# Performance work log

Hardware: AMD Instinct MI355X
Metric: run time of the kernel (lower is better)

## Reference

```python
import jax, jax.numpy as jnp
import numpy as np
import math

ANCHORS = np.array([[[10,13],[16,30],[33,23]],
                    [[30,61],[62,45],[59,119]],
                    [[116,90],[156,198],[373,326]]], dtype=np.float32)
STRIDES = [8.0, 16.0, 32.0]
BALANCE = [4.0, 1.0, 0.4]
LAMBDA_BOX, LAMBDA_OBJ, LAMBDA_CLS = 0.05, 1.0, 0.5
ANCHOR_T = 4.0
CP, CN = 1.0, 0.0  # label_smoothing = 0
EPS = 1e-7


def _bce(x, t):
    # BCEWithLogits, elementwise, numerically stable
    return jnp.maximum(x, 0.) - x * t + jnp.log1p(jnp.exp(-jnp.abs(x)))


def _ciou(b1, b2):
    # b1, b2: (M, 4) xyxy
    ix1 = jnp.maximum(b1[:, 0], b2[:, 0]); iy1 = jnp.maximum(b1[:, 1], b2[:, 1])
    ix2 = jnp.minimum(b1[:, 2], b2[:, 2]); iy2 = jnp.minimum(b1[:, 3], b2[:, 3])
    inter = jnp.clip(ix2 - ix1, 0.) * jnp.clip(iy2 - iy1, 0.)
    a1 = (b1[:, 2] - b1[:, 0]) * (b1[:, 3] - b1[:, 1])
    a2 = (b2[:, 2] - b2[:, 0]) * (b2[:, 3] - b2[:, 1])
    union = a1 + a2 - inter + EPS
    iou = inter / union
    ex1 = jnp.minimum(b1[:, 0], b2[:, 0]); ey1 = jnp.minimum(b1[:, 1], b2[:, 1])
    ex2 = jnp.maximum(b1[:, 2], b2[:, 2]); ey2 = jnp.maximum(b1[:, 3], b2[:, 3])
    c2 = (ex2 - ex1) ** 2 + (ey2 - ey1) ** 2 + EPS
    # center distance^2: centers are (x1+x2)/2
    rho2 = ((b1[:, 0] + b1[:, 2] - b2[:, 0] - b2[:, 2]) ** 2 +
            (b1[:, 1] + b1[:, 3] - b2[:, 1] - b2[:, 3]) ** 2) / 4.
    w1 = b1[:, 2] - b1[:, 0]; h1 = b1[:, 3] - b1[:, 1]
    w2 = b2[:, 2] - b2[:, 0]; h2 = b2[:, 3] - b2[:, 1]
    v = (4. / math.pi ** 2) * (jnp.arctan(w2 / (h2 + EPS)) - jnp.arctan(w1 / (h1 + EPS))) ** 2
    alpha = jax.lax.stop_gradient(v / (1. - iou + v + EPS))  # torch.no_grad()
    return iou - rho2 / c2 - alpha * v


def _layer_loss(pred, targets, anchor, balance):
    # pred: (B, na, H, W, 5+nc); targets: (nt, 6); anchor: (na, 2) in grid units
    B, na, H, W, C = pred.shape
    nc = C - 5
    nt = targets.shape[0]
    gain = jnp.array([1., 1., W, H, W, H], jnp.float32)
    t = targets * gain  # (nt, 6): [b, cls, gx, gy, gw, gh]
    # anchor-ratio filter
    r = t[:, 4:6][None] / (anchor[:, None] + 1e-16)            # (na, nt, 2)
    anchor_ok = jnp.max(jnp.maximum(r, 1. / r), axis=2) < ANCHOR_T  # (na, nt)
    # neighbor-cell selection masks (center + 4 neighbors)
    gxy = t[:, 2:4]
    gxi = jnp.floor(gxy)
    frac = gxy - gxi
    jm = (frac[:, 0] > .5) & (gxi[:, 0] < W - 1)
    km = (frac[:, 1] > .5) & (gxi[:, 1] < H - 1)
    lm = (frac[:, 0] < .5) & (gxi[:, 0] > 0)
    mm = (frac[:, 1] < .5) & (gxi[:, 1] > 0)
    sel = jnp.stack([jnp.ones_like(jm), jm, km, lm, mm])       # (5, nt)
    valid = sel[:, None, :] & anchor_ok[None]                  # (5, na, nt)
    off = jnp.array([[0, 0], [1, 0], [0, 1], [-1, 0], [0, -1]], jnp.float32)
    gxy_e = gxy[None] - off[:, None]                           # (5, nt, 2)
    gi = jnp.clip(jnp.floor(gxy_e).astype(jnp.int32), 0,
                  jnp.array([W - 1, H - 1], jnp.int32))        # (5, nt, 2)
    txy = gxy_e - gi.astype(jnp.float32)                       # offset-form xy
    gwh = t[:, 4:6]
    tbox = jnp.concatenate([txy - gwh[None] / 2., txy + gwh[None] / 2.], -1)  # (5, nt, 4)
    # flatten fixed-size candidate set (5 * na * nt), masked by `valid`
    shp = (5, na, nt)
    b_idx = jnp.broadcast_to(t[:, 0].astype(jnp.int32)[None, None], shp).reshape(-1)
    cls_i = jnp.broadcast_to(t[:, 1].astype(jnp.int32)[None, None], shp).reshape(-1)
    a_idx = jnp.broadcast_to(jnp.arange(na)[None, :, None], shp).reshape(-1)
    gx = jnp.broadcast_to(gi[:, None, :, 0], shp).reshape(-1)
    gy = jnp.broadcast_to(gi[:, None, :, 1], shp).reshape(-1)
    tbox_f = jnp.broadcast_to(tbox[:, None], shp + (4,)).reshape(-1, 4)
    vmask = valid.reshape(-1).astype(pred.dtype)
    cnt = vmask.sum()
    # fancy-indexed gather of matched predictions
    pm = pred[b_idx, a_idx, gy, gx]                            # (M, C)
    pxy = jax.nn.sigmoid(pm[:, :2]) * 2. - 0.5
    pwh = (jax.nn.sigmoid(pm[:, 2:4]) * 2.) ** 2 * anchor[a_idx]
    pbox = jnp.concatenate([pxy - pwh / 2., pxy + pwh / 2.], -1)
    ciou = _ciou(pbox, tbox_f)
    lbox = jnp.where(cnt > 0, jnp.sum((1. - ciou) * vmask) / jnp.maximum(cnt, 1.), 0.)
    # objectness target scatter (detached, clamped CIoU); invalid write 0 -> no-op under max
    tobj = jnp.zeros(pred.shape[:4], pred.dtype)
    vals = jax.lax.stop_gradient(jnp.clip(ciou, 0.) * vmask)
    tobj = tobj.at[b_idx, a_idx, gy, gx].max(vals)
    lobj = jnp.mean(_bce(pred[..., 4], tobj)) * balance
    # classification (mean over matched rows x nc elems)
    ct = CN + (CP - CN) * jax.nn.one_hot(cls_i, nc, dtype=pm.dtype)
    lcls = jnp.where(cnt > 0,
                     jnp.sum(_bce(pm[:, 5:], ct) * vmask[:, None]) / jnp.maximum(cnt * nc, 1.),
                     0.)
    return lbox, lobj, lcls


def _forward(pred0, pred1, pred2, targets):
    B = pred0.shape[0]
    preds = [pred0, pred1, pred2]
    lb = lo = lc = 0.
    for i in range(3):
        anchor = jnp.asarray(ANCHORS[i]) / STRIDES[i]
        bx, ob, cl = _layer_loss(preds[i], targets, anchor, BALANCE[i])
        lb = lb + bx; lo = lo + ob; lc = lc + cl
    return (LAMBDA_BOX * lb + LAMBDA_OBJ * lo + LAMBDA_CLS * lc) * B


def setup_inputs() -> dict:
    key = jax.random.key(0)
    ks = jax.random.split(key, 7)
    B, NT = 16, 300
    pred0 = jax.random.normal(ks[0], (B, 3, 80, 80, 85), jnp.float32)
    pred1 = jax.random.normal(ks[1], (B, 3, 40, 40, 85), jnp.float32)
    pred2 = jax.random.normal(ks[2], (B, 3, 20, 20, 85), jnp.float32)
    b = jax.random.randint(ks[3], (NT, 1), 0, B).astype(jnp.float32)
    c = jax.random.randint(ks[4], (NT, 1), 0, 80).astype(jnp.float32)
    cxy = jax.random.uniform(ks[5], (NT, 2), jnp.float32, 0.02, 0.98)
    wh = jax.random.uniform(ks[6], (NT, 2), jnp.float32, 0.02, 0.3)
    targets = jnp.concatenate([b, c, cxy, wh], axis=1)  # (NT, 6)
    return {"pred0": pred0, "pred1": pred1, "pred2": pred2, "targets": targets}


def reference(pred0, pred1, pred2, targets):
    return _forward(pred0, pred1, pred2, targets)
```

## Files before the change

kernel.cpp:

```cpp
#include <hip/hip_runtime.h>
#include <math.h>

#define EPSF 1e-7f
#define NT1 256
#define NT2 1024

__device__ __constant__ float d_anch[3][3][2] = {
    {{10.f/8.f,  13.f/8.f},  {16.f/8.f,  30.f/8.f},  {33.f/8.f,  23.f/8.f}},
    {{30.f/16.f, 61.f/16.f}, {62.f/16.f, 45.f/16.f}, {59.f/16.f, 119.f/16.f}},
    {{116.f/32.f,90.f/32.f}, {156.f/32.f,198.f/32.f},{373.f/32.f,326.f/32.f}},
};

__device__ __forceinline__ float bce0(float x) {
    return fmaxf(x, 0.0f) + log1pf(expf(-fabsf(x)));
}
__device__ __forceinline__ float bcef(float x, float t) {
    return fmaxf(x, 0.0f) - x * t + log1pf(expf(-fabsf(x)));
}
__device__ __forceinline__ float sigm(float x) {
    return 1.0f / (1.0f + expf(-x));
}

template <int NT>
__device__ __forceinline__ float block_reduce(float v, float* s) {
    s[threadIdx.x] = v;
    __syncthreads();
    for (int st = NT / 2; st > 0; st >>= 1) {
        if (threadIdx.x < st) s[threadIdx.x] += s[threadIdx.x + st];
        __syncthreads();
    }
    float r = s[0];
    __syncthreads();
    return r;
}

__global__ void stream_kernel(const float* __restrict__ pred0,
                              const float* __restrict__ pred1,
                              const float* __restrict__ pred2,
                              float* __restrict__ tobj,
                              float* __restrict__ objpart,
                              int n0, int n1, int n2)
{
    int idx = blockIdx.x * NT1 + threadIdx.x;
    int N = n0 + n1 + n2;
    float acc = 0.0f;
    if (idx < N) {
        tobj[idx] = 0.0f;
        const float* pred; int cell; float w;
        if (idx < n0)           { pred = pred0; cell = idx;            w = 4.0f / (float)n0; }
        else if (idx < n0 + n1) { pred = pred1; cell = idx - n0;       w = 1.0f / (float)n1; }
        else                    { pred = pred2; cell = idx - n0 - n1;  w = 0.4f / (float)n2; }
        float x = pred[(size_t)cell * 85 + 4];
        acc = w * bce0(x);
    }
    __shared__ float s[NT1];
    float r = block_reduce<NT1>(acc, s);
    if (threadIdx.x == 0) objpart[blockIdx.x] = r;
}

__global__ void entry_kernel(const float* __restrict__ pred0,
                             const float* __restrict__ pred1,
                             const float* __restrict__ pred2,
                             const float* __restrict__ targets,
                             int nt, int bpl2,
                             float* __restrict__ tobj_base,
                             float* __restrict__ blockpart,
                             int n0, int n1, int n2)
{
    int layer = blockIdx.x / bpl2;
    int sub   = blockIdx.x % bpl2;
    int wid   = threadIdx.x >> 6;
    int lane  = threadIdx.x & 63;
    int perLayer = 15 * nt;
    int eL = sub * 16 + wid;

    const float* pred; float* tobj; int H, W; float wl;
    if (layer == 0)      { pred = pred0; tobj = tobj_base;           H = 80; W = 80; wl = 4.0f / (float)n0; }
    else if (layer == 1) { pred = pred1; tobj = tobj_base + n0;      H = 40; W = 40; wl = 1.0f / (float)n1; }
    else                 { pred = pred2; tobj = tobj_base + n0 + n1; H = 20; W = 20; wl = 0.4f / (float)n2; }

    float lbox = 0.0f, cnt = 0.0f, corr = 0.0f, clsacc = 0.0f;

    if (eL < perLayer) {
        int t = eL % nt;
        int a = (eL / nt) % 3;
        int o = eL / (nt * 3);

        const float* tg = targets + t * 6;
        float tb = tg[0], tc = tg[1];
        float gx = tg[2] * (float)W, gy = tg[3] * (float)H;
        float gw = tg[4] * (float)W, gh = tg[5] * (float)H;

        float aw = d_anch[layer][a][0], ah = d_anch[layer][a][1];
        float rw = gw / (aw + 1e-16f), rh = gh / (ah + 1e-16f);
        float rmax = fmaxf(fmaxf(rw, 1.0f / rw), fmaxf(rh, 1.0f / rh));
        bool aok = rmax < 4.0f;

        float fxi = floorf(gx), fyi = floorf(gy);
        float fx = gx - fxi, fy = gy - fyi;
        bool selo;
        switch (o) {
            case 0: selo = true; break;
            case 1: selo = (fx > 0.5f) && (fxi < (float)(W - 1)); break;
            case 2: selo = (fy > 0.5f) && (fyi < (float)(H - 1)); break;
            case 3: selo = (fx < 0.5f) && (fxi > 0.0f); break;
            default: selo = (fy < 0.5f) && (fyi > 0.0f); break;
        }

        if (aok && selo) {
            float ox = (o == 1) ? 1.0f : (o == 3) ? -1.0f : 0.0f;
            float oy = (o == 2) ? 1.0f : (o == 4) ? -1.0f : 0.0f;
            float gex = gx - ox, gey = gy - oy;
            int gix = min(max((int)floorf(gex), 0), W - 1);
            int giy = min(max((int)floorf(gey), 0), H - 1);
            float txc = gex - (float)gix, tyc = gey - (float)giy;
            float tx1 = txc - gw * 0.5f, ty1 = tyc - gh * 0.5f;
            float tx2 = txc + gw * 0.5f, ty2 = tyc + gh * 0.5f;

            int b = (int)tb, cls = (int)tc;
            int cell = (int)(((((size_t)b * 3 + a) * H + giy) * W + gix));
            const float* pm = pred + (size_t)cell * 85;

            float p0 = pm[0], p1v = pm[1], p2v = pm[2], p3 = pm[3];
            float pxc = sigm(p0) * 2.0f - 0.5f;
            float pyc = sigm(p1v) * 2.0f - 0.5f;
            float sw = sigm(p2v) * 2.0f;
            float sh = sigm(p3) * 2.0f;
            float pw = sw * sw * aw, ph = sh * sh * ah;
            float px1 = pxc - pw * 0.5f, py1 = pyc - ph * 0.5f;
            float px2 = pxc + pw * 0.5f, py2 = pyc + ph * 0.5f;

            float ix1 = fmaxf(px1, tx1), iy1 = fmaxf(py1, ty1);
            float ix2 = fminf(px2, tx2), iy2 = fminf(py2, ty2);
            float inter = fmaxf(ix2 - ix1, 0.0f) * fmaxf(iy2 - iy1, 0.0f);
            float a1 = (px2 - px1) * (py2 - py1);
            float a2 = (tx2 - tx1) * (ty2 - ty1);
            float uni = a1 + a2 - inter + EPSF;
            float iou = inter / uni;
            float ex1 = fminf(px1, tx1), ey1 = fminf(py1, ty1);
            float ex2 = fmaxf(px2, tx2), ey2 = fmaxf(py2, ty2);
            float cw = ex2 - ex1, chh = ey2 - ey1;
            float c2 = cw * cw + chh * chh + EPSF;
            float dx = px1 + px2 - tx1 - tx2;
            float dy = py1 + py2 - ty1 - ty2;
            float rho2 = (dx * dx + dy * dy) * 0.25f;
            float w1 = px2 - px1, h1 = py2 - py1;
            float w2 = tx2 - tx1, h2 = ty2 - ty1;
            float dat = atanf(w2 / (h2 + EPSF)) - atanf(w1 / (h1 + EPSF));
            float v = 0.40528473f * dat * dat;
            float alpha = v / (1.0f - iou + v + EPSF);
            float ciou = iou - rho2 / c2 - alpha * v;

            if (lane == 0) {
                lbox = 1.0f - ciou;
                cnt = 1.0f;
                float vobj = fmaxf(ciou, 0.0f);
                unsigned int oldb = atomicMax((unsigned int*)&tobj[cell],
                                              __float_as_uint(vobj));
                float old = __uint_as_float(oldb);
                float nw = fmaxf(vobj, old);
                corr = wl * pm[4] * (nw - old);
            }

            float xc = pm[5 + lane];
            clsacc = bcef(xc, (lane == cls) ? 1.0f : 0.0f);
            if (lane < 16) {
                float xc2 = pm[69 + lane];
                clsacc += bcef(xc2, ((64 + lane) == cls) ? 1.0f : 0.0f);
            }
        }
    }

    __shared__ float s[NT2];
    float rb = block_reduce<NT2>(lbox, s);
    float rc = block_reduce<NT2>(cnt, s);
    float rl = block_reduce<NT2>(clsacc, s);
    float rr = block_reduce<NT2>(corr, s);
    if (threadIdx.x == 0) {
        float* p = blockpart + (size_t)blockIdx.x * 4;
        p[0] = rb; p[1] = rc; p[2] = rl; p[3] = rr;
    }
}

__global__ void final_kernel(const float* __restrict__ objpart, int nb1,
                             const float* __restrict__ blockpart, int bpl2,
                             float* __restrict__ out, int B)
{
    __shared__ float s[NT1];
    int tid = threadIdx.x;

    float v = 0.0f;
    for (int i = tid; i < nb1; i += NT1) v += objpart[i];
    float objsum = block_reduce<NT1>(v, s);

    float corrsum;
    {
        float v2 = 0.0f;
        int nbk = 3 * bpl2;
        for (int i = tid; i < nbk; i += NT1) v2 += blockpart[(size_t)i * 4 + 3];
        corrsum = block_reduce<NT1>(v2, s);
    }

    float r_lb[3], r_cnt[3], r_cls[3];
    for (int L = 0; L < 3; ++L) {
        float v2 = 0.0f;
        for (int i = tid; i < bpl2; i += NT1) v2 += blockpart[(size_t)(L * bpl2 + i) * 4 + 0];
        r_lb[L] = block_reduce<NT1>(v2, s);
        v2 = 0.0f;
        for (int i = tid; i < bpl2; i += NT1) v2 += blockpart[(size_t)(L * bpl2 + i) * 4 + 1];
        r_cnt[L] = block_reduce<NT1>(v2, s);
        v2 = 0.0f;
        for (int i = tid; i < bpl2; i += NT1) v2 += blockpart[(size_t)(L * bpl2 + i) * 4 + 2];
        r_cls[L] = block_reduce<NT1>(v2, s);
    }

    if (tid == 0) {
        float lobj = objsum - corrsum;
        float lb = 0.0f, lc = 0.0f;
        for (int L = 0; L < 3; ++L) {
            if (r_cnt[L] > 0.0f) {
                lb += r_lb[L] / fmaxf(r_cnt[L], 1.0f);
                lc += r_cls[L] / fmaxf(r_cnt[L] * 80.0f, 1.0f);
            }
        }
        out[0] = (0.05f * lb + lobj + 0.5f * lc) * (float)B;
    }
}

extern "C" void kernel_launch(void* const* d_in, const int* in_sizes, int n_in,
                              void* d_out, int out_size, void* d_ws, size_t ws_size,
                              hipStream_t stream) {
    const float* pred0 = (const float*)d_in[0];
    const float* pred1 = (const float*)d_in[1];
    const float* pred2 = (const float*)d_in[2];
    const float* targets = (const float*)d_in[3];

    int B = in_sizes[0] / (3 * 80 * 80 * 85);
    int nt = in_sizes[3] / 6;
    int n0 = B * 3 * 80 * 80;
    int n1 = B * 3 * 40 * 40;
    int n2 = B * 3 * 20 * 20;
    int N = n0 + n1 + n2;
    int NB1 = (N + NT1 - 1) / NT1;
    int perLayer = 15 * nt;
    int bpl2 = (perLayer + 15) / 16;
    int grid2 = 3 * bpl2;

    float* tobj = (float*)d_ws;
    float* objpart = tobj + N;
    float* blockpart = objpart + NB1;

    stream_kernel<<<NB1, NT1, 0, stream>>>(
        pred0, pred1, pred2, tobj, objpart, n0, n1, n2);
    entry_kernel<<<grid2, NT2, 0, stream>>>(
        pred0, pred1, pred2, targets, nt, bpl2, tobj, blockpart, n0, n1, n2);
    final_kernel<<<1, NT1, 0, stream>>>(
        objpart, NB1, blockpart, bpl2, (float*)d_out, B);
}
```

Before: 45.34 us.

## Fuse objectness sweep into entry kernel and split tobj zeroing out

Moves the tobj zeroing into a separate float4-vectorized zero kernel. The objectness BCE sweep and the per-target entry work now run as two block ranges inside one fused launch, and each block writes a five-value partial. This lets the strided objectness reads overlap with the gather-heavy target blocks, and the sweep now uses 1024-thread blocks. In exchange the sweep blocks run five block reductions instead of one, which adds barrier overhead. The zero kernel also assumes N is divisible by 4.

```diff
diff --git a/kernel.cpp b/kernel.cpp
--- a/kernel.cpp
+++ b/kernel.cpp
@@ -2,8 +2,8 @@
 #include <math.h>
 
 #define EPSF 1e-7f
-#define NT1 256
-#define NT2 1024
+#define NT 1024
+#define NTF 256
 
 __device__ __constant__ float d_anch[3][3][2] = {
     {{10.f/8.f,  13.f/8.f},  {16.f/8.f,  30.f/8.f},  {33.f/8.f,  23.f/8.f}},
@@ -21,11 +21,11 @@
     return 1.0f / (1.0f + expf(-x));
 }
 
-template <int NT>
+template <int NTH>
 __device__ __forceinline__ float block_reduce(float v, float* s) {
     s[threadIdx.x] = v;
     __syncthreads();
-    for (int st = NT / 2; st > 0; st >>= 1) {
+    for (int st = NTH / 2; st > 0; st >>= 1) {
         if (threadIdx.x < st) s[threadIdx.x] += s[threadIdx.x + st];
         __syncthreads();
     }
@@ -34,184 +34,178 @@
     return r;
 }
 
-__global__ void stream_kernel(const float* __restrict__ pred0,
-                              const float* __restrict__ pred1,
-                              const float* __restrict__ pred2,
-                              float* __restrict__ tobj,
-                              float* __restrict__ objpart,
-                              int n0, int n1, int n2)
+__global__ void zero_kernel(float4* __restrict__ p, int n4)
 {
-    int idx = blockIdx.x * NT1 + threadIdx.x;
-    int N = n0 + n1 + n2;
-    float acc = 0.0f;
-    if (idx < N) {
-        tobj[idx] = 0.0f;
-        const float* pred; int cell; float w;
-        if (idx < n0)           { pred = pred0; cell = idx;            w = 4.0f / (float)n0; }
-        else if (idx < n0 + n1) { pred = pred1; cell = idx - n0;       w = 1.0f / (float)n1; }
-        else                    { pred = pred2; cell = idx - n0 - n1;  w = 0.4f / (float)n2; }
-        float x = pred[(size_t)cell * 85 + 4];
-        acc = w * bce0(x);
-    }
-    __shared__ float s[NT1];
-    float r = block_reduce<NT1>(acc, s);
-    if (threadIdx.x == 0) objpart[blockIdx.x] = r;
-}
-
-__global__ void entry_kernel(const float* __restrict__ pred0,
+    int i = blockIdx.x * NT + threadIdx.x;
+    if (i < n4) p[i] = make_float4(0.f, 0.f, 0.f, 0.f);
+}
+
+__global__ void fused_kernel(const float* __restrict__ pred0,
                              const float* __restrict__ pred1,
                              const float* __restrict__ pred2,
                              const float* __restrict__ targets,
-                             int nt, int bpl2,
+                             int nt, int sweepBlocks, int bpl2,
                              float* __restrict__ tobj_base,
                              float* __restrict__ blockpart,
                              int n0, int n1, int n2)
 {
-    int layer = blockIdx.x / bpl2;
-    int sub   = blockIdx.x % bpl2;
-    int wid   = threadIdx.x >> 6;
-    int lane  = threadIdx.x & 63;
-    int perLayer = 15 * nt;
-    int eL = sub * 16 + wid;
-
-    const float* pred; float* tobj; int H, W; float wl;
-    if (layer == 0)      { pred = pred0; tobj = tobj_base;           H = 80; W = 80; wl = 4.0f / (float)n0; }
-    else if (layer == 1) { pred = pred1; tobj = tobj_base + n0;      H = 40; W = 40; wl = 1.0f / (float)n1; }
-    else                 { pred = pred2; tobj = tobj_base + n0 + n1; H = 20; W = 20; wl = 0.4f / (float)n2; }
-
-    float lbox = 0.0f, cnt = 0.0f, corr = 0.0f, clsacc = 0.0f;
-
-    if (eL < perLayer) {
-        int t = eL % nt;
-        int a = (eL / nt) % 3;
-        int o = eL / (nt * 3);
-
-        const float* tg = targets + t * 6;
-        float tb = tg[0], tc = tg[1];
-        float gx = tg[2] * (float)W, gy = tg[3] * (float)H;
-        float gw = tg[4] * (float)W, gh = tg[5] * (float)H;
-
-        float aw = d_anch[layer][a][0], ah = d_anch[layer][a][1];
-        float rw = gw / (aw + 1e-16f), rh = gh / (ah + 1e-16f);
-        float rmax = fmaxf(fmaxf(rw, 1.0f / rw), fmaxf(rh, 1.0f / rh));
-        bool aok = rmax < 4.0f;
-
-        float fxi = floorf(gx), fyi = floorf(gy);
-        float fx = gx - fxi, fy = gy - fyi;
-        bool selo;
-        switch (o) {
-            case 0: selo = true; break;
-            case 1: selo = (fx > 0.5f) && (fxi < (float)(W - 1)); break;
-            case 2: selo = (fy > 0.5f) && (fyi < (float)(H - 1)); break;
-            case 3: selo = (fx < 0.5f) && (fxi > 0.0f); break;
-            default: selo = (fy < 0.5f) && (fyi > 0.0f); break;
+    float lbox = 0.0f, cnt = 0.0f, corr = 0.0f, clsacc = 0.0f, objacc = 0.0f;
+
+    if (blockIdx.x < sweepBlocks) {
+        int idx = blockIdx.x * NT + threadIdx.x;
+        int N = n0 + n1 + n2;
+        if (idx < N) {
+            const float* pred; int cell; float w;
+            if (idx < n0)           { pred = pred0; cell = idx;           w = 4.0f / (float)n0; }
+            else if (idx < n0 + n1) { pred = pred1; cell = idx - n0;      w = 1.0f / (float)n1; }
+            else                    { pred = pred2; cell = idx - n0 - n1; w = 0.4f / (float)n2; }
+            objacc = w * bce0(pred[(size_t)cell * 85 + 4]);
         }
-
-        if (aok && selo) {
-            float ox = (o == 1) ? 1.0f : (o == 3) ? -1.0f : 0.0f;
-            float oy = (o == 2) ? 1.0f : (o == 4) ? -1.0f : 0.0f;
-            float gex = gx - ox, gey = gy - oy;
-            int gix = min(max((int)floorf(gex), 0), W - 1);
-            int giy = min(max((int)floorf(gey), 0), H - 1);
-            float txc = gex - (float)gix, tyc = gey - (float)giy;
-            float tx1 = txc - gw * 0.5f, ty1 = tyc - gh * 0.5f;
-            float tx2 = txc + gw * 0.5f, ty2 = tyc + gh * 0.5f;
-
-            int b = (int)tb, cls = (int)tc;
-            int cell = (int)(((((size_t)b * 3 + a) * H + giy) * W + gix));
-            const float* pm = pred + (size_t)cell * 85;
-
-            float p0 = pm[0], p1v = pm[1], p2v = pm[2], p3 = pm[3];
-            float pxc = sigm(p0) * 2.0f - 0.5f;
-            float pyc = sigm(p1v) * 2.0f - 0.5f;
-            float sw = sigm(p2v) * 2.0f;
-            float sh = sigm(p3) * 2.0f;
-            float pw = sw * sw * aw, ph = sh * sh * ah;
-            float px1 = pxc - pw * 0.5f, py1 = pyc - ph * 0.5f;
-            float px2 = pxc + pw * 0.5f, py2 = pyc + ph * 0.5f;
-
-            float ix1 = fmaxf(px1, tx1), iy1 = fmaxf(py1, ty1);
-            float ix2 = fminf(px2, tx2), iy2 = fminf(py2, ty2);
-            float inter = fmaxf(ix2 - ix1, 0.0f) * fmaxf(iy2 - iy1, 0.0f);
-            float a1 = (px2 - px1) * (py2 - py1);
-            float a2 = (tx2 - tx1) * (ty2 - ty1);
-            float uni = a1 + a2 - inter + EPSF;
-            float iou = inter / uni;
-            float ex1 = fminf(px1, tx1), ey1 = fminf(py1, ty1);
-            float ex2 = fmaxf(px2, tx2), ey2 = fmaxf(py2, ty2);
-            float cw = ex2 - ex1, chh = ey2 - ey1;
-            float c2 = cw * cw + chh * chh + EPSF;
-            float dx = px1 + px2 - tx1 - tx2;
-            float dy = py1 + py2 - ty1 - ty2;
-            float rho2 = (dx * dx + dy * dy) * 0.25f;
-            float w1 = px2 - px1, h1 = py2 - py1;
-            float w2 = tx2 - tx1, h2 = ty2 - ty1;
-            float dat = atanf(w2 / (h2 + EPSF)) - atanf(w1 / (h1 + EPSF));
-            float v = 0.40528473f * dat * dat;
-            float alpha = v / (1.0f - iou + v + EPSF);
-            float ciou = iou - rho2 / c2 - alpha * v;
-
-            if (lane == 0) {
-                lbox = 1.0f - ciou;
-                cnt = 1.0f;
-                float vobj = fmaxf(ciou, 0.0f);
-                unsigned int oldb = atomicMax((unsigned int*)&tobj[cell],
-                                              __float_as_uint(vobj));
-                float old = __uint_as_float(oldb);
-                float nw = fmaxf(vobj, old);
-                corr = wl * pm[4] * (nw - old);
+    } else {
+        int eb    = blockIdx.x - sweepBlocks;
+        int layer = eb / bpl2;
+        int sub   = eb % bpl2;
+        int wid   = threadIdx.x >> 6;
+        int lane  = threadIdx.x & 63;
+        int perLayer = 15 * nt;
+        int eL = sub * 16 + wid;
+
+        const float* pred; float* tobj; int H, W; float wl;
+        if (layer == 0)      { pred = pred0; tobj = tobj_base;           H = 80; W = 80; wl = 4.0f / (float)n0; }
+        else if (layer == 1) { pred = pred1; tobj = tobj_base + n0;      H = 40; W = 40; wl = 1.0f / (float)n1; }
+        else                 { pred = pred2; tobj = tobj_base + n0 + n1; H = 20; W = 20; wl = 0.4f / (float)n2; }
+
+        if (eL < perLayer) {
+            int t = eL % nt;
+            int a = (eL / nt) % 3;
+            int o = eL / (nt * 3);
+
+            const float* tg = targets + t * 6;
+            float tb = tg[0], tc = tg[1];
+            float gx = tg[2] * (float)W, gy = tg[3] * (float)H;
+            float gw = tg[4] * (float)W, gh = tg[5] * (float)H;
+
+            float aw = d_anch[layer][a][0], ah = d_anch[layer][a][1];
+            float rw = gw / (aw + 1e-16f), rh = gh / (ah + 1e-16f);
+            float rmax = fmaxf(fmaxf(rw, 1.0f / rw), fmaxf(rh, 1.0f / rh));
+            bool aok = rmax < 4.0f;
+
+            float fxi = floorf(gx), fyi = floorf(gy);
+            float fx = gx - fxi, fy = gy - fyi;
+            bool selo;
+            switch (o) {
+                case 0: selo = true; break;
+                case 1: selo = (fx > 0.5f) && (fxi < (float)(W - 1)); break;
+                case 2: selo = (fy > 0.5f) && (fyi < (float)(H - 1)); break;
+                case 3: selo = (fx < 0.5f) && (fxi > 0.0f); break;
+                default: selo = (fy < 0.5f) && (fyi > 0.0f); break;
             }
 
-            float xc = pm[5 + lane];
-            clsacc = bcef(xc, (lane == cls) ? 1.0f : 0.0f);
-            if (lane < 16) {
-                float xc2 = pm[69 + lane];
-                clsacc += bcef(xc2, ((64 + lane) == cls) ? 1.0f : 0.0f);
+            if (aok && selo) {
+                float ox = (o == 1) ? 1.0f : (o == 3) ? -1.0f : 0.0f;
+                float oy = (o == 2) ? 1.0f : (o == 4) ? -1.0f : 0.0f;
+                float gex = gx - ox, gey = gy - oy;
+                int gix = min(max((int)floorf(gex), 0), W - 1);
+                int giy = min(max((int)floorf(gey), 0), H - 1);
+                float txc = gex - (float)gix, tyc = gey - (float)giy;
+                float tx1 = txc - gw * 0.5f, ty1 = tyc - gh * 0.5f;
+                float tx2 = txc + gw * 0.5f, ty2 = tyc + gh * 0.5f;
+
+                int b = (int)tb, cls = (int)tc;
+                int cell = (int)(((((size_t)b * 3 + a) * H + giy) * W + gix));
+                const float* pm = pred + (size_t)cell * 85;
+
+                float p0 = pm[0], p1v = pm[1], p2v = pm[2], p3 = pm[3];
+                float pxc = sigm(p0) * 2.0f - 0.5f;
+                float pyc = sigm(p1v) * 2.0f - 0.5f;
+                float sw = sigm(p2v) * 2.0f;
+                float sh = sigm(p3) * 2.0f;
+                float pw = sw * sw * aw, ph = sh * sh * ah;
+                float px1 = pxc - pw * 0.5f, py1 = pyc - ph * 0.5f;
+                float px2 = pxc + pw * 0.5f, py2 = pyc + ph * 0.5f;
+
+                float ix1 = fmaxf(px1, tx1), iy1 = fmaxf(py1, ty1);
+                float ix2 = fminf(px2, tx2), iy2 = fminf(py2, ty2);
+                float inter = fmaxf(ix2 - ix1, 0.0f) * fmaxf(iy2 - iy1, 0.0f);
+                float a1 = (px2 - px1) * (py2 - py1);
+                float a2 = (tx2 - tx1) * (ty2 - ty1);
+                float uni = a1 + a2 - inter + EPSF;
+                float iou = inter / uni;
+                float ex1 = fminf(px1, tx1), ey1 = fminf(py1, ty1);
+                float ex2 = fmaxf(px2, tx2), ey2 = fmaxf(py2, ty2);
+                float cw = ex2 - ex1, chh = ey2 - ey1;
+                float c2 = cw * cw + chh * chh + EPSF;
+                float dx = px1 + px2 - tx1 - tx2;
+                float dy = py1 + py2 - ty1 - ty2;
+                float rho2 = (dx * dx + dy * dy) * 0.25f;
+                float w1 = px2 - px1, h1 = py2 - py1;
+                float w2 = tx2 - tx1, h2 = ty2 - ty1;
+                float dat = atanf(w2 / (h2 + EPSF)) - atanf(w1 / (h1 + EPSF));
+                float v = 0.40528473f * dat * dat;
+                float alpha = v / (1.0f - iou + v + EPSF);
+                float ciou = iou - rho2 / c2 - alpha * v;
+
+                if (lane == 0) {
+                    lbox = 1.0f - ciou;
+                    cnt = 1.0f;
+                    float vobj = fmaxf(ciou, 0.0f);
+                    unsigned int oldb = atomicMax((unsigned int*)&tobj[cell],
+                                                  __float_as_uint(vobj));
+                    float old = __uint_as_float(oldb);
+                    float nw = fmaxf(vobj, old);
+                    corr = wl * pm[4] * (nw - old);
+                }
+
+                float xc = pm[5 + lane];
+                clsacc = bcef(xc, (lane == cls) ? 1.0f : 0.0f);
+                if (lane < 16) {
+                    float xc2 = pm[69 + lane];
+                    clsacc += bcef(xc2, ((64 + lane) == cls) ? 1.0f : 0.0f);
+                }
             }
         }
     }
 
-    __shared__ float s[NT2];
-    float rb = block_reduce<NT2>(lbox, s);
-    float rc = block_reduce<NT2>(cnt, s);
-    float rl = block_reduce<NT2>(clsacc, s);
-    float rr = block_reduce<NT2>(corr, s);
+    __shared__ float s[NT];
+    float rb = block_reduce<NT>(lbox, s);
+    float rc = block_reduce<NT>(cnt, s);
+    float rl = block_reduce<NT>(clsacc, s);
+    float rr = block_reduce<NT>(corr, s);
+    float ro = block_reduce<NT>(objacc, s);
     if (threadIdx.x == 0) {
-        float* p = blockpart + (size_t)blockIdx.x * 4;
-        p[0] = rb; p[1] = rc; p[2] = rl; p[3] = rr;
-    }
-}
-
-__global__ void final_kernel(const float* __restrict__ objpart, int nb1,
-                             const float* __restrict__ blockpart, int bpl2,
+        float* p = blockpart + (size_t)blockIdx.x * 5;
+        p[0] = rb; p[1] = rc; p[2] = rl; p[3] = rr; p[4] = ro;
+    }
+}
+
+__global__ void final_kernel(const float* __restrict__ blockpart,
+                             int sweepBlocks, int bpl2,
                              float* __restrict__ out, int B)
 {
-    __shared__ float s[NT1];
+    __shared__ float s[NTF];
     int tid = threadIdx.x;
+    int total = sweepBlocks + 3 * bpl2;
 
     float v = 0.0f;
-    for (int i = tid; i < nb1; i += NT1) v += objpart[i];
-    float objsum = block_reduce<NT1>(v, s);
-
-    float corrsum;
-    {
-        float v2 = 0.0f;
-        int nbk = 3 * bpl2;
-        for (int i = tid; i < nbk; i += NT1) v2 += blockpart[(size_t)i * 4 + 3];
-        corrsum = block_reduce<NT1>(v2, s);
-    }
+    for (int i = tid; i < total; i += NTF) v += blockpart[(size_t)i * 5 + 4];
+    float objsum = block_reduce<NTF>(v, s);
+
+    v = 0.0f;
+    for (int i = tid; i < total; i += NTF) v += blockpart[(size_t)i * 5 + 3];
+    float corrsum = block_reduce<NTF>(v, s);
 
     float r_lb[3], r_cnt[3], r_cls[3];
     for (int L = 0; L < 3; ++L) {
+        const float* base = blockpart + (size_t)(sweepBlocks + L * bpl2) * 5;
         float v2 = 0.0f;
-        for (int i = tid; i < bpl2; i += NT1) v2 += blockpart[(size_t)(L * bpl2 + i) * 4 + 0];
-        r_lb[L] = block_reduce<NT1>(v2, s);
+        for (int i = tid; i < bpl2; i += NTF) v2 += base[(size_t)i * 5 + 0];
+        r_lb[L] = block_reduce<NTF>(v2, s);
         v2 = 0.0f;
-        for (int i = tid; i < bpl2; i += NT1) v2 += blockpart[(size_t)(L * bpl2 + i) * 4 + 1];
-        r_cnt[L] = block_reduce<NT1>(v2, s);
+        for (int i = tid; i < bpl2; i += NTF) v2 += base[(size_t)i * 5 + 1];
+        r_cnt[L] = block_reduce<NTF>(v2, s);
         v2 = 0.0f;
-        for (int i = tid; i < bpl2; i += NT1) v2 += blockpart[(size_t)(L * bpl2 + i) * 4 + 2];
-        r_cls[L] = block_reduce<NT1>(v2, s);
+        for (int i = tid; i < bpl2; i += NTF) v2 += base[(size_t)i * 5 + 2];
+        r_cls[L] = block_reduce<NTF>(v2, s);
     }
 
     if (tid == 0) {
@@ -241,19 +235,19 @@
     int n1 = B * 3 * 40 * 40;
     int n2 = B * 3 * 20 * 20;
     int N = n0 + n1 + n2;
-    int NB1 = (N + NT1 - 1) / NT1;
     int perLayer = 15 * nt;
+    int sweepBlocks = (N + NT - 1) / NT;
     int bpl2 = (perLayer + 15) / 16;
-    int grid2 = 3 * bpl2;
+    int grid2 = sweepBlocks + 3 * bpl2;
 
     float* tobj = (float*)d_ws;
-    float* objpart = tobj + N;
-    float* blockpart = objpart + NB1;
-
-    stream_kernel<<<NB1, NT1, 0, stream>>>(
-        pred0, pred1, pred2, tobj, objpart, n0, n1, n2);
-    entry_kernel<<<grid2, NT2, 0, stream>>>(
-        pred0, pred1, pred2, targets, nt, bpl2, tobj, blockpart, n0, n1, n2);
-    final_kernel<<<1, NT1, 0, stream>>>(
-        objpart, NB1, blockpart, bpl2, (float*)d_out, B);
-}
+    float* blockpart = tobj + N;
+
+    int n4 = N / 4;
+    zero_kernel<<<(n4 + NT - 1) / NT, NT, 0, stream>>>((float4*)tobj, n4);
+    fused_kernel<<<grid2, NT, 0, stream>>>(
+        pred0, pred1, pred2, targets, nt, sweepBlocks, bpl2,
+        tobj, blockpart, n0, n1, n2);
+    final_kernel<<<1, NTF, 0, stream>>>(
+        blockpart, sweepBlocks, bpl2, (float*)d_out, B);
+}
```

New measurement: 47.54 us. 1.05x slower.

## Replace shared-memory tree reductions with wave shuffles and shrink block sizes

Applied to the files above, without the earlier changes.

Swaps the barrier-heavy shared-memory tree reduction for 64-lane shuffle reductions followed by a small per-wave shared combine, in all three kernels. The stream kernel now has each thread handle four cells, so it launches a quarter as many blocks. The entry kernel drops from 1024 to 256 threads, with one entry per wave kept, which gives four times as many blocks. The aim is to cut the many __syncthreads rounds and the partial-sum traffic, at the cost of more partial results for the final kernel to sum.

```diff
diff --git a/kernel.cpp b/kernel.cpp
--- a/kernel.cpp
+++ b/kernel.cpp
@@ -2,8 +2,7 @@
 #include <math.h>
 
 #define EPSF 1e-7f
-#define NT1 256
-#define NT2 1024
+#define NT 256
 
 __device__ __constant__ float d_anch[3][3][2] = {
     {{10.f/8.f,  13.f/8.f},  {16.f/8.f,  30.f/8.f},  {33.f/8.f,  23.f/8.f}},
@@ -21,58 +20,59 @@
     return 1.0f / (1.0f + expf(-x));
 }
 
-template <int NT>
-__device__ __forceinline__ float block_reduce(float v, float* s) {
-    s[threadIdx.x] = v;
-    __syncthreads();
-    for (int st = NT / 2; st > 0; st >>= 1) {
-        if (threadIdx.x < st) s[threadIdx.x] += s[threadIdx.x + st];
-        __syncthreads();
-    }
-    float r = s[0];
-    __syncthreads();
-    return r;
-}
-
-__global__ void stream_kernel(const float* __restrict__ pred0,
-                              const float* __restrict__ pred1,
-                              const float* __restrict__ pred2,
-                              float* __restrict__ tobj,
-                              float* __restrict__ objpart,
-                              int n0, int n1, int n2)
+__device__ __forceinline__ float wave_reduce(float v) {
+    #pragma unroll
+    for (int off = 32; off > 0; off >>= 1) v += __shfl_down(v, off, 64);
+    return v;
+}
+
+__global__ void __launch_bounds__(NT)
+stream_kernel(const float* __restrict__ pred0,
+              const float* __restrict__ pred1,
+              const float* __restrict__ pred2,
+              float* __restrict__ tobj,
+              float* __restrict__ objpart,
+              int n0, int n1, int n2)
 {
-    int idx = blockIdx.x * NT1 + threadIdx.x;
     int N = n0 + n1 + n2;
+    int base = blockIdx.x * (NT * 4) + threadIdx.x;
     float acc = 0.0f;
-    if (idx < N) {
-        tobj[idx] = 0.0f;
-        const float* pred; int cell; float w;
-        if (idx < n0)           { pred = pred0; cell = idx;            w = 4.0f / (float)n0; }
-        else if (idx < n0 + n1) { pred = pred1; cell = idx - n0;       w = 1.0f / (float)n1; }
-        else                    { pred = pred2; cell = idx - n0 - n1;  w = 0.4f / (float)n2; }
-        float x = pred[(size_t)cell * 85 + 4];
-        acc = w * bce0(x);
-    }
-    __shared__ float s[NT1];
-    float r = block_reduce<NT1>(acc, s);
-    if (threadIdx.x == 0) objpart[blockIdx.x] = r;
-}
-
-__global__ void entry_kernel(const float* __restrict__ pred0,
-                             const float* __restrict__ pred1,
-                             const float* __restrict__ pred2,
-                             const float* __restrict__ targets,
-                             int nt, int bpl2,
-                             float* __restrict__ tobj_base,
-                             float* __restrict__ blockpart,
-                             int n0, int n1, int n2)
+    #pragma unroll
+    for (int k = 0; k < 4; ++k) {
+        int idx = base + k * NT;
+        if (idx < N) {
+            tobj[idx] = 0.0f;
+            const float* pred; int cell; float w;
+            if (idx < n0)           { pred = pred0; cell = idx;           w = 4.0f / (float)n0; }
+            else if (idx < n0 + n1) { pred = pred1; cell = idx - n0;      w = 1.0f / (float)n1; }
+            else                    { pred = pred2; cell = idx - n0 - n1; w = 0.4f / (float)n2; }
+            acc += w * bce0(pred[(size_t)cell * 85 + 4]);
+        }
+    }
+    __shared__ float s[4];
+    float r = wave_reduce(acc);
+    if ((threadIdx.x & 63) == 0) s[threadIdx.x >> 6] = r;
+    __syncthreads();
+    if (threadIdx.x == 0)
+        objpart[blockIdx.x] = s[0] + s[1] + s[2] + s[3];
+}
+
+__global__ void __launch_bounds__(NT)
+entry_kernel(const float* __restrict__ pred0,
+             const float* __restrict__ pred1,
+             const float* __restrict__ pred2,
+             const float* __restrict__ targets,
+             int nt, int bpl,
+             float* __restrict__ tobj_base,
+             float* __restrict__ blockpart,
+             int n0, int n1, int n2)
 {
-    int layer = blockIdx.x / bpl2;
-    int sub   = blockIdx.x % bpl2;
+    int layer = blockIdx.x / bpl;
+    int sub   = blockIdx.x % bpl;
     int wid   = threadIdx.x >> 6;
     int lane  = threadIdx.x & 63;
     int perLayer = 15 * nt;
-    int eL = sub * 16 + wid;
+    int eL = sub * 4 + wid;
 
     const float* pred; float* tobj; int H, W; float wl;
     if (layer == 0)      { pred = pred0; tobj = tobj_base;           H = 80; W = 80; wl = 4.0f / (float)n0; }
@@ -171,56 +171,70 @@
         }
     }
 
-    __shared__ float s[NT2];
-    float rb = block_reduce<NT2>(lbox, s);
-    float rc = block_reduce<NT2>(cnt, s);
-    float rl = block_reduce<NT2>(clsacc, s);
-    float rr = block_reduce<NT2>(corr, s);
-    if (threadIdx.x == 0) {
-        float* p = blockpart + (size_t)blockIdx.x * 4;
-        p[0] = rb; p[1] = rc; p[2] = rl; p[3] = rr;
-    }
-}
-
-__global__ void final_kernel(const float* __restrict__ objpart, int nb1,
-                             const float* __restrict__ blockpart, int bpl2,
-                             float* __restrict__ out, int B)
+    float rb = wave_reduce(lbox);
+    float rc = wave_reduce(cnt);
+    float rl = wave_reduce(clsacc);
+    float rr = wave_reduce(corr);
+    __shared__ float s[4][4];
+    if (lane == 0) {
+        s[wid][0] = rb; s[wid][1] = rc; s[wid][2] = rl; s[wid][3] = rr;
+    }
+    __syncthreads();
+    if (threadIdx.x < 4) {
+        float v = s[0][threadIdx.x] + s[1][threadIdx.x] +
+                  s[2][threadIdx.x] + s[3][threadIdx.x];
+        blockpart[(size_t)blockIdx.x * 4 + threadIdx.x] = v;
+    }
+}
+
+__global__ void __launch_bounds__(NT)
+final_kernel(const float* __restrict__ objpart, int nb1,
+             const float* __restrict__ blockpart, int bpl,
+             float* __restrict__ out, int B)
 {
-    __shared__ float s[NT1];
+    __shared__ float s[4];
+    __shared__ float comp[11];
     int tid = threadIdx.x;
+    int lane = tid & 63;
+    int wid = tid >> 6;
 
     float v = 0.0f;
-    for (int i = tid; i < nb1; i += NT1) v += objpart[i];
-    float objsum = block_reduce<NT1>(v, s);
-
-    float corrsum;
-    {
-        float v2 = 0.0f;
-        int nbk = 3 * bpl2;
-        for (int i = tid; i < nbk; i += NT1) v2 += blockpart[(size_t)i * 4 + 3];
-        corrsum = block_reduce<NT1>(v2, s);
-    }
-
-    float r_lb[3], r_cnt[3], r_cls[3];
-    for (int L = 0; L < 3; ++L) {
-        float v2 = 0.0f;
-        for (int i = tid; i < bpl2; i += NT1) v2 += blockpart[(size_t)(L * bpl2 + i) * 4 + 0];
-        r_lb[L] = block_reduce<NT1>(v2, s);
-        v2 = 0.0f;
-        for (int i = tid; i < bpl2; i += NT1) v2 += blockpart[(size_t)(L * bpl2 + i) * 4 + 1];
-        r_cnt[L] = block_reduce<NT1>(v2, s);
-        v2 = 0.0f;
-        for (int i = tid; i < bpl2; i += NT1) v2 += blockpart[(size_t)(L * bpl2 + i) * 4 + 2];
-        r_cls[L] = block_reduce<NT1>(v2, s);
+    for (int i = tid; i < nb1; i += NT) v += objpart[i];
+    v = wave_reduce(v);
+    if (lane == 0) s[wid] = v;
+    __syncthreads();
+    if (tid == 0) comp[9] = s[0] + s[1] + s[2] + s[3];
+    __syncthreads();
+
+    for (int c = 0; c < 4; ++c) {
+        for (int L = 0; L < 3; ++L) {
+            float v2 = 0.0f;
+            if (c < 3) {
+                for (int i = tid; i < bpl; i += NT)
+                    v2 += blockpart[(size_t)(L * bpl + i) * 4 + c];
+            } else if (L == 0) {
+                for (int i = tid; i < 3 * bpl; i += NT)
+                    v2 += blockpart[(size_t)i * 4 + 3];
+            } else continue;
+            v2 = wave_reduce(v2);
+            if (lane == 0) s[wid] = v2;
+            __syncthreads();
+            if (tid == 0) {
+                float r = s[0] + s[1] + s[2] + s[3];
+                if (c < 3) comp[L * 3 + c] = r; else comp[10] = r;
+            }
+            __syncthreads();
+        }
     }
 
     if (tid == 0) {
-        float lobj = objsum - corrsum;
+        float lobj = comp[9] - comp[10];
         float lb = 0.0f, lc = 0.0f;
         for (int L = 0; L < 3; ++L) {
-            if (r_cnt[L] > 0.0f) {
-                lb += r_lb[L] / fmaxf(r_cnt[L], 1.0f);
-                lc += r_cls[L] / fmaxf(r_cnt[L] * 80.0f, 1.0f);
+            float cb = comp[L * 3 + 0], cc = comp[L * 3 + 1], cl = comp[L * 3 + 2];
+            if (cc > 0.0f) {
+                lb += cb / fmaxf(cc, 1.0f);
+                lc += cl / fmaxf(cc * 80.0f, 1.0f);
             }
         }
         out[0] = (0.05f * lb + lobj + 0.5f * lc) * (float)B;
@@ -241,19 +255,19 @@
     int n1 = B * 3 * 40 * 40;
     int n2 = B * 3 * 20 * 20;
     int N = n0 + n1 + n2;
-    int NB1 = (N + NT1 - 1) / NT1;
+    int NB1 = (N + NT * 4 - 1) / (NT * 4);
     int perLayer = 15 * nt;
-    int bpl2 = (perLayer + 15) / 16;
-    int grid2 = 3 * bpl2;
+    int bpl = (perLayer + 3) / 4;
+    int grid2 = 3 * bpl;
 
     float* tobj = (float*)d_ws;
     float* objpart = tobj + N;
     float* blockpart = objpart + NB1;
 
-    stream_kernel<<<NB1, NT1, 0, stream>>>(
+    stream_kernel<<<NB1, NT, 0, stream>>>(
         pred0, pred1, pred2, tobj, objpart, n0, n1, n2);
-    entry_kernel<<<grid2, NT2, 0, stream>>>(
-        pred0, pred1, pred2, targets, nt, bpl2, tobj, blockpart, n0, n1, n2);
-    final_kernel<<<1, NT1, 0, stream>>>(
-        objpart, NB1, blockpart, bpl2, (float*)d_out, B);
-}
+    entry_kernel<<<grid2, NT, 0, stream>>>(
+        pred0, pred1, pred2, targets, nt, bpl, tobj, blockpart, n0, n1, n2);
+    final_kernel<<<1, NT, 0, stream>>>(
+        objpart, NB1, blockpart, bpl, (float*)d_out, B);
+}
```

After: 41.41 us. -8.7%, faster.
